# Optimization experiments

Measured on AMD Instinct MI355X. Metric: run time of the kernel, lower is better.

Reference implementation:

```python
import jax, jax.numpy as jnp
import numpy as np

N_NODES = 100000
N_EDGES = 1600000
F_IN, F1, F2, F3 = 128, 128, 128, 64


def setup_inputs() -> dict:
    key = jax.random.key(0)
    ks = jax.random.split(key, 10)
    edge_index = jax.random.randint(ks[0], (2, N_EDGES), 0, N_NODES, dtype=jnp.int64)
    x = jax.random.normal(ks[1], (N_NODES, F_IN), dtype=jnp.float32)
    def glorot(k, fi, fo):
        s = (6.0 / (fi + fo)) ** 0.5
        return jax.random.uniform(k, (fi, fo), jnp.float32, -s, s)
    return {
        "edge_index": edge_index,
        "x": x,
        "W1": glorot(ks[2], F_IN, F1), "b1": jnp.zeros((F1,), jnp.float32),
        "W2": glorot(ks[3], F1, F2), "b2": jnp.zeros((F2,), jnp.float32),
        "W3": glorot(ks[4], F2, F3), "b3": jnp.zeros((F3,), jnp.float32),
        "W_att": glorot(ks[5], F3, F3),
    }


def _gcn_conv(x, W, b, src, dst, deg_inv_sqrt):
    h = x @ W  # [N, Fo]
    norm = deg_inv_sqrt[src] * deg_inv_sqrt[dst]  # [E]
    agg = jax.ops.segment_sum(h[src] * norm[:, None], dst, num_segments=x.shape[0])
    agg = agg + h * (deg_inv_sqrt * deg_inv_sqrt)[:, None]  # self-loop term
    return agg + b


def _attention_pool(emb, W_att):
    # SimGNN attention pooling
    ctx = jnp.tanh(jnp.mean(emb @ W_att, axis=0))          # [F3]
    scores = jax.nn.sigmoid(emb @ ctx)                      # [N]
    return emb.T @ scores[:, None]                          # [F3, 1]


def reference(edge_index, x, W1, b1, W2, b2, W3, b3, W_att):
    src, dst = edge_index[0], edge_index[1]
    n = x.shape[0]
    deg = jax.ops.segment_sum(jnp.ones_like(src, dtype=x.dtype), dst, num_segments=n) + 1.0
    dis = jax.lax.rsqrt(deg)
    h = jax.nn.relu(_gcn_conv(x, W1, b1, src, dst, dis))
    h = jax.nn.relu(_gcn_conv(h, W2, b2, src, dst, dis))
    h = _gcn_conv(h, W3, b3, src, dst, dis)                 # abstract_features [N, F3]
    pooled = _attention_pool(h, W_att)                      # [F3, 1]
    return h, pooled
```

## Files before the change

kernel.cpp:

```cpp
#include <hip/hip_runtime.h>
#include <hip/hip_bf16.h>

#define NN 100000
#define NE 1600000
#define NR 100032
#define NB2 196
#define NBLK 391
#define EPB 4096

#if defined(__has_builtin)
#  if __has_builtin(__builtin_amdgcn_cvt_pk_f32_fp8) && \
      __has_builtin(__builtin_amdgcn_cvt_pk_fp8_f32) && \
      __has_builtin(__builtin_amdgcn_cvt_f32_fp8)
#    define HWF8 1
#  endif
#endif

typedef float f32x2 __attribute__((ext_vector_type(2)));
typedef float f32x4 __attribute__((ext_vector_type(4)));
typedef short bf16x8 __attribute__((ext_vector_type(8)));

static __device__ __forceinline__ float bf2f(__hip_bfloat16 v) { return __bfloat162float(v); }
static __device__ __forceinline__ float bfu(unsigned short w) {
    return __uint_as_float((unsigned)w << 16);
}

static __device__ __forceinline__ float f8d_sw(unsigned b) {
    unsigned e = (b >> 3) & 15u, m = b & 7u;
    float mag;
    if (e == 0) mag = (float)m * 0.001953125f;
    else        mag = __uint_as_float(((e + 120u) << 23) | (m << 20));
    return (b & 0x80u) ? -mag : mag;
}
static __device__ __forceinline__ unsigned char f8e_sw(float x) {
    unsigned u = __float_as_uint(x);
    unsigned s = (u >> 31) << 7;
    unsigned au = u & 0x7fffffffu;
    if (au >= 0x43E00000u) return (unsigned char)(s | 0x7Eu);
    if (au <  0x3A800000u) return (unsigned char)s;
    if (au <  0x3C800000u) {
        float a = __uint_as_float(au);
        int m = (int)rintf(a * 512.0f);
        if (m >= 8) return (unsigned char)(s | 0x08u);
        return (unsigned char)(s | (unsigned)m);
    }
    au += 0x80000u;
    if (au >= 0x43E00000u) return (unsigned char)(s | 0x7Eu);
    unsigned e = (au >> 23) - 120u;
    unsigned m = (au >> 20) & 7u;
    return (unsigned char)(s | (e << 3) | m);
}

static __device__ __forceinline__ void f8d4(unsigned u, float* o) {
#ifdef HWF8
    f32x2 lo = __builtin_amdgcn_cvt_pk_f32_fp8((int)u, false);
    f32x2 hi = __builtin_amdgcn_cvt_pk_f32_fp8((int)u, true);
    o[0] = lo.x; o[1] = lo.y; o[2] = hi.x; o[3] = hi.y;
#else
    o[0] = f8d_sw(u & 255u); o[1] = f8d_sw((u >> 8) & 255u);
    o[2] = f8d_sw((u >> 16) & 255u); o[3] = f8d_sw(u >> 24);
#endif
}
static __device__ __forceinline__ unsigned short f8e2(float a, float b) {
#ifdef HWF8
    float ca = fminf(fmaxf(a, -448.0f), 448.0f);
    float cb = fminf(fmaxf(b, -448.0f), 448.0f);
    int p = __builtin_amdgcn_cvt_pk_fp8_f32(ca, cb, 0, false);
    return (unsigned short)(p & 0xFFFF);
#else
    return (unsigned short)f8e_sw(a) | ((unsigned short)f8e_sw(b) << 8);
#endif
}
static __device__ __forceinline__ unsigned bfpack(float lo, float hi) {
    return (__float_as_uint(lo) >> 16) | (__float_as_uint(hi) & 0xFFFF0000u);
}

static __device__ __forceinline__ void acc8_add(f32x2* acc, uint2 v) {
#ifdef HWF8
    acc[0] += __builtin_amdgcn_cvt_pk_f32_fp8((int)v.x, false);
    acc[1] += __builtin_amdgcn_cvt_pk_f32_fp8((int)v.x, true);
    acc[2] += __builtin_amdgcn_cvt_pk_f32_fp8((int)v.y, false);
    acc[3] += __builtin_amdgcn_cvt_pk_f32_fp8((int)v.y, true);
#else
    unsigned u[2] = {v.x, v.y};
#pragma unroll
    for (int q = 0; q < 2; q++) {
        float o[4]; f8d4(u[q], o);
        acc[2 * q]     += (f32x2){o[0], o[1]};
        acc[2 * q + 1] += (f32x2){o[2], o[3]};
    }
#endif
}

__global__ void k_probe1(const unsigned short* __restrict__ xw,
                         const int* __restrict__ ei, int* __restrict__ raw) {
    int i = blockIdx.x * 256 + threadIdx.x;
    int nan = ((xw[i] & 0x7F80u) == 0x7F80u) ? 1 : 0;
    int odd = (ei[2 * i + 1] != 0) ? 1 : 0;
    unsigned long long bn = __ballot(nan);
    unsigned long long bo = __ballot(odd);
    if ((threadIdx.x & 63) == 0) {
        if (bn) atomicAdd(&raw[0], __popcll(bn));
        if (bo) atomicAdd(&raw[1], __popcll(bo));
    }
}

static __device__ __forceinline__ int e_src(const int* ei, int e, int f64) {
    int v = f64 ? ei[2 * e] : ei[e];
    return min(max(v, 0), NN - 1);
}
static __device__ __forceinline__ int e_dst(const int* ei, int e, int f64) {
    int v = f64 ? ei[2 * (NE + e)] : ei[NE + e];
    return min(max(v, 0), NN - 1);
}
static __device__ __forceinline__ float ldx(const void* p, long long i, int f32) {
    return f32 ? ((const float*)p)[i] : bf2f(((const __hip_bfloat16*)p)[i]);
}

__global__ __launch_bounds__(256) void k_prep(const void* __restrict__ x,
                                              const void* W1, const void* b1,
                                              const void* W2, const void* b2,
                                              const void* W3, const void* b3,
                                              const void* Wa,
                                              unsigned short* W1b, unsigned short* W2b,
                                              unsigned short* W3b,
                                              float* b1f, float* b2f, float* b3f,
                                              float* Waf,
                                              unsigned char* __restrict__ P,
                                              const int* __restrict__ raw,
                                              float* colsum, float* pooled, int* wsync) {
    int t = threadIdx.x;
    int gi = blockIdx.x;
    int f = raw[0] > 0;
    if (gi < 12500) {
        int i = gi * 256 + t;
        unsigned pk;
        if (f) {
            float4 v = ((const float4*)x)[i];
            pk = (unsigned)f8e2(v.x, v.y) | ((unsigned)f8e2(v.z, v.w) << 16);
        } else {
            ushort4 v = ((const ushort4*)x)[i];
            pk = (unsigned)f8e2(bfu(v.x), bfu(v.y)) | ((unsigned)f8e2(bfu(v.z), bfu(v.w)) << 16);
        }
        ((unsigned*)P)[i] = pk;
        return;
    }
    int i = (gi - 12500) * 256 + t;
    {
        int j = i & 7, l = (i >> 3) & 63, c = (i >> 9) & 7, kc = i >> 12;
        int k = kc * 32 + ((l >> 4)) * 8 + j;
        int col = c * 16 + (l & 15);
        W1b[i] = __bfloat16_as_ushort(__float2bfloat16(ldx(W1, k * 128 + col, f)));
        W2b[i] = __bfloat16_as_ushort(__float2bfloat16(ldx(W2, k * 128 + col, f)));
    }
    if (i < 8192) {
        int j = i & 7, l = (i >> 3) & 63, c = (i >> 9) & 3, kc = i >> 11;
        int k = kc * 32 + ((l >> 4)) * 8 + j;
        int col = c * 16 + (l & 15);
        W3b[i] = __bfloat16_as_ushort(__float2bfloat16(ldx(W3, k * 64 + col, f)));
    }
    if (i < 4096)  Waf[i] = ldx(Wa, i, f);
    if (i < 128)   { b1f[i] = ldx(b1, i, f); b2f[i] = ldx(b2, i, f); }
    if (i < 64)    b3f[i] = ldx(b3, i, f);
    if (gi == 12500) {
        if (t < 64) { colsum[t] = 0.0f; pooled[t] = 0.0f; }
        if (t == 0) *wsync = 0;
    }
    if (gi == 12501) {
        for (int z = t; z < (NR - NN) * 32; z += 256)
            ((unsigned*)(P + (size_t)NN * 128))[z] = 0u;
    }
}

__global__ __launch_bounds__(256) void k_hist(const int* __restrict__ ei,
                                              int* __restrict__ ghist,
                                              const int* __restrict__ raw) {
    __shared__ int h[NB2];
    int blk = blockIdx.x, t = threadIdx.x;
    for (int i = t; i < NB2; i += 256) h[i] = 0;
    __syncthreads();
    int f64 = (raw[1] == 0);
    int e0 = blk * EPB;
    for (int i = t; i < EPB; i += 256) {
        int e = e0 + i;
        if (e < NE) atomicAdd(&h[e_dst(ei, e, f64) >> 9], 1);
    }
    __syncthreads();
    for (int i = t; i < NB2; i += 256) ghist[blk * NB2 + i] = h[i];
}

__global__ __launch_bounds__(256) void k_off(const int* __restrict__ ghist,
                                             int* __restrict__ cbase,
                                             int* __restrict__ offm,
                                             int* __restrict__ rowptr) {
    __shared__ int tot[NB2];
    int t = threadIdx.x;
    if (t < NB2) {
        int s = 0;
        for (int blk = 0; blk < NBLK; blk++) s += ghist[blk * NB2 + t];
        tot[t] = s;
    }
    __syncthreads();
    if (t == 0) {
        int run = 0;
        for (int b = 0; b < NB2; b++) { cbase[b] = run; run += tot[b]; }
        cbase[NB2] = run;
        rowptr[NN] = run;
    }
    __syncthreads();
    if (t < NB2) {
        int run = cbase[t];
        for (int blk = 0; blk < NBLK; blk++) {
            offm[blk * NB2 + t] = run;
            run += ghist[blk * NB2 + t];
        }
    }
}

__global__ __launch_bounds__(256) void k_scatter(const int* __restrict__ ei,
                                                 const int* __restrict__ offm,
                                                 int* __restrict__ scratch,
                                                 const int* __restrict__ raw) {
    __shared__ int cur[NB2];
    int blk = blockIdx.x, t = threadIdx.x;
    for (int i = t; i < NB2; i += 256) cur[i] = offm[blk * NB2 + i];
    __syncthreads();
    int f64 = (raw[1] == 0);
    int e0 = blk * EPB;
    for (int i = t; i < EPB; i += 256) {
        int e = e0 + i;
        if (e < NE) {
            int d = e_dst(ei, e, f64);
            int s = e_src(ei, e, f64);
            int p = atomicAdd(&cur[d >> 9], 1);
            p = min(max(p, 0), NE - 1);
            scratch[p] = s | ((d & 511) << 17);
        }
    }
}

__global__ __launch_bounds__(256) void k_build(const int* __restrict__ scratch,
                                               const int* __restrict__ cbase,
                                               int* __restrict__ rowptr,
                                               float* __restrict__ dis,
                                               int* __restrict__ csr) {
    __shared__ int hist[512];
    __shared__ int base[512];
    __shared__ int sd[256];
    int b = blockIdx.x, t = threadIdx.x;
    int n0 = b << 9;
    int s0 = cbase[b], s1 = cbase[b + 1];
    hist[t] = 0; hist[t + 256] = 0;
    __syncthreads();
    for (int i = s0 + t; i < s1; i += 256) {
        int dlo = (scratch[i] >> 17) & 511;
        atomicAdd(&hist[dlo], 1);
    }
    __syncthreads();
    int v0 = hist[2 * t], v1 = hist[2 * t + 1];
    int s = v0 + v1;
    sd[t] = s; __syncthreads();
    for (int o = 1; o < 256; o <<= 1) {
        int add = (t >= o) ? sd[t - o] : 0;
        __syncthreads();
        sd[t] += add;
        __syncthreads();
    }
    int run = s0 + sd[t] - s;
    base[2 * t] = run;
    base[2 * t + 1] = run + v0;
    int n = n0 + 2 * t;
    if (n < NN) {
        rowptr[n] = run;
        dis[n] = rsqrtf((float)v0 + 1.0f);
    }
    if (n + 1 < NN) {
        rowptr[n + 1] = run + v0;
        dis[n + 1] = rsqrtf((float)v1 + 1.0f);
    }
    __syncthreads();
    for (int i = s0 + t; i < s1; i += 256) {
        int v = scratch[i];
        int dlo = (v >> 17) & 511;
        int p = atomicAdd(&base[dlo], 1);
        p = min(max(p, 0), NE - 1);
        csr[p] = v & 0x1FFFF;
    }
}

template <int NCT>
__global__ __launch_bounds__(256) void k_xf_mfma(const unsigned char* __restrict__ A,
                                                 const unsigned short* __restrict__ Wf,
                                                 const float* __restrict__ dis,
                                                 unsigned char* __restrict__ O) {
    __shared__ unsigned short wl[NCT * 4 * 64 * 8];
    int t = threadIdx.x;
    int n0 = blockIdx.x * 64;
    {
        const uint4* wg = (const uint4*)Wf;
        uint4* wld = (uint4*)wl;
#pragma unroll
        for (int i = 0; i < NCT; i++) wld[i * 256 + t] = wg[i * 256 + t];
    }
    __syncthreads();
    int w = t >> 6, l = t & 63;
    int quad = l >> 4, m = l & 15;
    int node = n0 + w * 16 + m;
    const unsigned char* ap = A + (size_t)node * 128 + quad * 8;
    f32x4 acc[NCT];
#pragma unroll
    for (int c = 0; c < NCT; c++) acc[c] = (f32x4){0.0f, 0.0f, 0.0f, 0.0f};
#pragma unroll
    for (int kc = 0; kc < 4; kc++) {
        uint2 g = *(const uint2*)(ap + kc * 32);
        float o[8];
        f8d4(g.x, o); f8d4(g.y, o + 4);
        union { unsigned u[4]; bf16x8 v; } fr;
        fr.u[0] = bfpack(o[0], o[1]);
        fr.u[1] = bfpack(o[2], o[3]);
        fr.u[2] = bfpack(o[4], o[5]);
        fr.u[3] = bfpack(o[6], o[7]);
#pragma unroll
        for (int c = 0; c < NCT; c++) {
            bf16x8 bw = *(const bf16x8*)&wl[((kc * NCT + c) * 64 + l) * 8];
            acc[c] = __builtin_amdgcn_mfma_f32_16x16x32_bf16(bw, fr.v, acc[c], 0, 0, 0);
        }
    }
    float d = (node < NN) ? dis[node] : 0.0f;
    if (node <= NN) {
        unsigned char* orow = O + (size_t)node * (NCT * 16) + quad * 4;
#pragma unroll
        for (int c = 0; c < NCT; c++) {
            unsigned pk = (unsigned)f8e2(acc[c][0] * d, acc[c][1] * d)
                        | ((unsigned)f8e2(acc[c][2] * d, acc[c][3] * d) << 16);
            *(unsigned*)(orow + c * 16) = pk;
        }
    }
}

template <bool RELU>
__global__ __launch_bounds__(256) void k_agg128(const unsigned char* __restrict__ Tb,
                                                const int* __restrict__ rowptr,
                                                const int* __restrict__ csr,
                                                const float* __restrict__ dis,
                                                const float* __restrict__ bias,
                                                unsigned char* __restrict__ H) {
    int n = blockIdx.x * 4 + (threadIdx.x >> 6);
    int lane = threadIdx.x & 63;
    int r = lane >> 4;
    int f = lane & 15;
    int fo = f << 3;
    float dn = dis[n];
    int s0 = rowptr[n], s1 = rowptr[n + 1];
    s0 = min(max(s0, 0), NE); s1 = min(max(s1, s0), NE);
    f32x2 acc[4];
#pragma unroll
    for (int k = 0; k < 4; k++) acc[k] = (f32x2){0.0f, 0.0f};
    if (r == 0) {
        uint2 v = *(const uint2*)(Tb + (((unsigned)n << 7) + (unsigned)fo));
        acc8_add(acc, v);
    }
    for (int base = s0; base < s1; base += 64) {
        int m = min(64, s1 - base);
        unsigned voff = (unsigned)NN << 7;
        if (lane < m) voff = (unsigned)csr[base + lane] << 7;
        int nq = (m + 15) >> 4;
        for (int q = 0; q < nq; q++) {
            int a0 = q * 64 + r * 4;
            unsigned vo0 = (unsigned)__builtin_amdgcn_ds_bpermute(a0,      (int)voff);
            unsigned vo1 = (unsigned)__builtin_amdgcn_ds_bpermute(a0 + 16, (int)voff);
            unsigned vo2 = (unsigned)__builtin_amdgcn_ds_bpermute(a0 + 32, (int)voff);
            unsigned vo3 = (unsigned)__builtin_amdgcn_ds_bpermute(a0 + 48, (int)voff);
            uint2 v0 = *(const uint2*)(Tb + (vo0 + (unsigned)fo));
            uint2 v1 = *(const uint2*)(Tb + (vo1 + (unsigned)fo));
            uint2 v2 = *(const uint2*)(Tb + (vo2 + (unsigned)fo));
            uint2 v3 = *(const uint2*)(Tb + (vo3 + (unsigned)fo));
            acc8_add(acc, v0);
            acc8_add(acc, v1);
            acc8_add(acc, v2);
            acc8_add(acc, v3);
        }
    }
#pragma unroll
    for (int k = 0; k < 4; k++) {
        acc[k].x += __shfl_xor(acc[k].x, 16, 64);
        acc[k].y += __shfl_xor(acc[k].y, 16, 64);
        acc[k].x += __shfl_xor(acc[k].x, 32, 64);
        acc[k].y += __shfl_xor(acc[k].y, 32, 64);
    }
    if (r == 0) {
        float4 bA = *(const float4*)(bias + fo);
        float4 bB = *(const float4*)(bias + fo + 4);
        float t[8];
        t[0] = acc[0].x * dn + bA.x; t[1] = acc[0].y * dn + bA.y;
        t[2] = acc[1].x * dn + bA.z; t[3] = acc[1].y * dn + bA.w;
        t[4] = acc[2].x * dn + bB.x; t[5] = acc[2].y * dn + bB.y;
        t[6] = acc[3].x * dn + bB.z; t[7] = acc[3].y * dn + bB.w;
        if (RELU) {
#pragma unroll
            for (int k = 0; k < 8; k++) t[k] = fmaxf(t[k], 0.0f);
        }
        unsigned lo = (unsigned)f8e2(t[0], t[1]) | ((unsigned)f8e2(t[2], t[3]) << 16);
        unsigned hi = (unsigned)f8e2(t[4], t[5]) | ((unsigned)f8e2(t[6], t[7]) << 16);
        *(uint2*)(H + (((size_t)n << 7) + (size_t)fo)) = make_uint2(lo, hi);
    }
}

__global__ __launch_bounds__(256) void k_agg64(const unsigned char* __restrict__ Tb,
                                               const int* __restrict__ rowptr,
                                               const int* __restrict__ csr,
                                               const float* __restrict__ dis,
                                               const float* __restrict__ bias,
                                               unsigned short* __restrict__ Hb) {
    int lane = threadIdx.x & 63;
    int half = lane >> 5;
    int hl = lane & 31;
    int n = blockIdx.x * 8 + (threadIdx.x >> 6) * 2 + half;
    int r = hl >> 3;
    int f = hl & 7;
    int fo = f << 3;
    float dn = dis[n];
    int s0 = rowptr[n], s1 = rowptr[n + 1];
    s0 = min(max(s0, 0), NE); s1 = min(max(s1, s0), NE);
    f32x2 acc[4];
#pragma unroll
    for (int k = 0; k < 4; k++) acc[k] = (f32x2){0.0f, 0.0f};
    if (r == 0) {
        uint2 v = *(const uint2*)(Tb + (((unsigned)n << 6) + (unsigned)fo));
        acc8_add(acc, v);
    }
    int ab = half << 7;
    for (int base = s0; base < s1; base += 32) {
        int m = min(32, s1 - base);
        unsigned voff = (unsigned)NN << 6;
        if (hl < m) voff = (unsigned)csr[base + hl] << 6;
        int nq = (m + 15) >> 4;
        for (int q = 0; q < nq; q++) {
            int a0 = ab + q * 64 + r * 4;
            unsigned vo0 = (unsigned)__builtin_amdgcn_ds_bpermute(a0,      (int)voff);
            unsigned vo1 = (unsigned)__builtin_amdgcn_ds_bpermute(a0 + 16, (int)voff);
            unsigned vo2 = (unsigned)__builtin_amdgcn_ds_bpermute(a0 + 32, (int)voff);
            unsigned vo3 = (unsigned)__builtin_amdgcn_ds_bpermute(a0 + 48, (int)voff);
            uint2 v0 = *(const uint2*)(Tb + (vo0 + (unsigned)fo));
            uint2 v1 = *(const uint2*)(Tb + (vo1 + (unsigned)fo));
            uint2 v2 = *(const uint2*)(Tb + (vo2 + (unsigned)fo));
            uint2 v3 = *(const uint2*)(Tb + (vo3 + (unsigned)fo));
            acc8_add(acc, v0);
            acc8_add(acc, v1);
            acc8_add(acc, v2);
            acc8_add(acc, v3);
        }
    }
#pragma unroll
    for (int k = 0; k < 4; k++) {
        acc[k].x += __shfl_xor(acc[k].x, 8, 64);
        acc[k].y += __shfl_xor(acc[k].y, 8, 64);
        acc[k].x += __shfl_xor(acc[k].x, 16, 64);
        acc[k].y += __shfl_xor(acc[k].y, 16, 64);
    }
    if (r == 0) {
        float4 bA = *(const float4*)(bias + fo);
        float4 bB = *(const float4*)(bias + fo + 4);
        float t[8];
        t[0] = acc[0].x * dn + bA.x; t[1] = acc[0].y * dn + bA.y;
        t[2] = acc[1].x * dn + bA.z; t[3] = acc[1].y * dn + bA.w;
        t[4] = acc[2].x * dn + bB.x; t[5] = acc[2].y * dn + bB.y;
        t[6] = acc[3].x * dn + bB.z; t[7] = acc[3].y * dn + bB.w;
        unsigned p0 = (unsigned)__bfloat16_as_ushort(__float2bfloat16(t[0])) |
                      ((unsigned)__bfloat16_as_ushort(__float2bfloat16(t[1])) << 16);
        unsigned p1 = (unsigned)__bfloat16_as_ushort(__float2bfloat16(t[2])) |
                      ((unsigned)__bfloat16_as_ushort(__float2bfloat16(t[3])) << 16);
        unsigned p2 = (unsigned)__bfloat16_as_ushort(__float2bfloat16(t[4])) |
                      ((unsigned)__bfloat16_as_ushort(__float2bfloat16(t[5])) << 16);
        unsigned p3 = (unsigned)__bfloat16_as_ushort(__float2bfloat16(t[6])) |
                      ((unsigned)__bfloat16_as_ushort(__float2bfloat16(t[7])) << 16);
        *(uint4*)(Hb + (((size_t)n << 6) + (size_t)fo)) = make_uint4(p0, p1, p2, p3);
    }
}

__global__ __launch_bounds__(512) void k_colsum(const unsigned short* __restrict__ h3,
                                                float* __restrict__ colsum,
                                                const float* __restrict__ Waf,
                                                float* __restrict__ ctx,
                                                int* __restrict__ wsync) {
    int t = threadIdx.x;
    int lane = t & 63;
    int rg = lane >> 4, cq = lane & 15;
    int wid = (blockIdx.x * 512 + t) >> 6;
    int nw = (gridDim.x * 512) >> 6;
    float a0 = 0, a1 = 0, a2 = 0, a3 = 0;
    for (int r = wid * 4 + rg; r < NN; r += nw * 4) {
        uint2 v = *(const uint2*)(h3 + ((size_t)r << 6) + cq * 4);
        a0 += bfu((unsigned short)(v.x & 0xFFFF));
        a1 += bfu((unsigned short)(v.x >> 16));
        a2 += bfu((unsigned short)(v.y & 0xFFFF));
        a3 += bfu((unsigned short)(v.y >> 16));
    }
    a0 += __shfl_xor(a0, 16, 64); a0 += __shfl_xor(a0, 32, 64);
    a1 += __shfl_xor(a1, 16, 64); a1 += __shfl_xor(a1, 32, 64);
    a2 += __shfl_xor(a2, 16, 64); a2 += __shfl_xor(a2, 32, 64);
    a3 += __shfl_xor(a3, 16, 64); a3 += __shfl_xor(a3, 32, 64);
    __shared__ float part[8][64];
    int w = t >> 6;
    if (rg == 0) {
        part[w][cq * 4 + 0] = a0;
        part[w][cq * 4 + 1] = a1;
        part[w][cq * 4 + 2] = a2;
        part[w][cq * 4 + 3] = a3;
    }
    __syncthreads();
    if (t < 64) {
        float s = 0;
#pragma unroll
        for (int i = 0; i < 8; i++) s += part[i][t];
        atomicAdd(&colsum[t], s);
    }
    __shared__ int lastf;
    __syncthreads();
    if (t == 0) {
        __threadfence();
        int old = atomicAdd(wsync, 1);
        lastf = (old == (int)gridDim.x - 1) ? 1 : 0;
    }
    __syncthreads();
    if (lastf) {
        __shared__ float ms[64];
        if (t < 64) {
            __threadfence();
            ms[t] = atomicAdd(&colsum[t], 0.0f) * (1.0f / NN);
        }
        __syncthreads();
        if (t < 64) {
            float s = 0.0f;
#pragma unroll
            for (int k = 0; k < 64; k++) s += ms[k] * Waf[k * 64 + t];
            ctx[t] = tanhf(s);
        }
    }
}

__global__ __launch_bounds__(512) void k_pool(const unsigned short* __restrict__ h3,
                                              const float* __restrict__ ctx,
                                              float* __restrict__ pooled,
                                              void* __restrict__ out,
                                              const int* __restrict__ raw) {
    int t = threadIdx.x;
    int lane = t & 63;
    int rg = lane >> 4, cq = lane & 15;
    int wid = (blockIdx.x * 512 + t) >> 6;
    int nw = (gridDim.x * 512) >> 6;
    int f32o = raw[0] > 0;
    float c0 = ctx[cq * 4 + 0], c1 = ctx[cq * 4 + 1];
    float c2 = ctx[cq * 4 + 2], c3 = ctx[cq * 4 + 3];
    float q0 = 0, q1 = 0, q2 = 0, q3 = 0;
    for (int r = wid * 4 + rg; r < NN; r += nw * 4) {
        uint2 v = *(const uint2*)(h3 + ((size_t)r << 6) + cq * 4);
        float x0 = bfu((unsigned short)(v.x & 0xFFFF));
        float x1 = bfu((unsigned short)(v.x >> 16));
        float x2 = bfu((unsigned short)(v.y & 0xFFFF));
        float x3 = bfu((unsigned short)(v.y >> 16));
        if (f32o) {
            *(float4*)((float*)out + ((size_t)r << 6) + cq * 4) =
                make_float4(x0, x1, x2, x3);
        } else {
            *(uint2*)((unsigned short*)out + ((size_t)r << 6) + cq * 4) = v;
        }
        float p = x0 * c0 + x1 * c1 + x2 * c2 + x3 * c3;
        p += __shfl_xor(p, 1, 64);
        p += __shfl_xor(p, 2, 64);
        p += __shfl_xor(p, 4, 64);
        p += __shfl_xor(p, 8, 64);
        float sc = 1.0f / (1.0f + expf(-p));
        q0 += sc * x0; q1 += sc * x1; q2 += sc * x2; q3 += sc * x3;
    }
    q0 += __shfl_xor(q0, 16, 64); q0 += __shfl_xor(q0, 32, 64);
    q1 += __shfl_xor(q1, 16, 64); q1 += __shfl_xor(q1, 32, 64);
    q2 += __shfl_xor(q2, 16, 64); q2 += __shfl_xor(q2, 32, 64);
    q3 += __shfl_xor(q3, 16, 64); q3 += __shfl_xor(q3, 32, 64);
    __shared__ float part[8][64];
    int w = t >> 6;
    if (rg == 0) {
        part[w][cq * 4 + 0] = q0;
        part[w][cq * 4 + 1] = q1;
        part[w][cq * 4 + 2] = q2;
        part[w][cq * 4 + 3] = q3;
    }
    __syncthreads();
    if (t < 64) {
        float s = 0;
#pragma unroll
        for (int i = 0; i < 8; i++) s += part[i][t];
        atomicAdd(&pooled[t], s);
    }
}

__global__ void k_tail(const float* __restrict__ pooled, void* __restrict__ out,
                       const int* __restrict__ raw) {
    int j = threadIdx.x;
    if (raw[0] > 0) {
        ((float*)out)[6400000 + j] = pooled[j];
    } else {
        ((unsigned short*)out)[6400000 + j] =
            __bfloat16_as_ushort(__float2bfloat16(pooled[j]));
    }
}

static constexpr size_t AL(size_t x) { return (x + 255) & ~size_t(255); }
static constexpr size_t OFF_FLAGS  = 0;
static constexpr size_t OFF_RAW    = OFF_FLAGS + 256;
static constexpr size_t OFF_GHIST  = OFF_RAW + 256;
static constexpr size_t OFF_OFFM   = OFF_GHIST + AL((size_t)NBLK * NB2 * 4);
static constexpr size_t OFF_CBASE  = OFF_OFFM + AL((size_t)NBLK * NB2 * 4);
static constexpr size_t OFF_ROWPTR = OFF_CBASE + AL((NB2 + 1) * 4);
static constexpr size_t OFF_CSR    = OFF_ROWPTR + AL((NN + 1) * 4);
static constexpr size_t OFF_DIS    = OFF_CSR + AL((size_t)NE * 4);
static constexpr size_t OFF_P      = OFF_DIS + AL(NN * 4);
static constexpr size_t OFF_W1B    = OFF_P + AL((size_t)NR * 128);
static constexpr size_t OFF_W2B    = OFF_W1B + AL(16384 * 2);
static constexpr size_t OFF_W3B    = OFF_W2B + AL(16384 * 2);
static constexpr size_t OFF_B1F    = OFF_W3B + AL(8192 * 2);
static constexpr size_t OFF_B2F    = OFF_B1F + AL(128 * 4);
static constexpr size_t OFF_B3F    = OFF_B2F + AL(128 * 4);
static constexpr size_t OFF_WAF    = OFF_B3F + AL(64 * 4);
static constexpr size_t OFF_COLSUM = OFF_WAF + AL(4096 * 4);
static constexpr size_t OFF_POOLED = OFF_COLSUM + AL(64 * 4);
static constexpr size_t OFF_CTX    = OFF_POOLED + AL(64 * 4);
static constexpr size_t OFF_SYNC   = OFF_CTX + AL(64 * 4);

extern "C" void kernel_launch(void* const* d_in, const int* in_sizes, int n_in,
                              void* d_out, int out_size, void* d_ws, size_t ws_size,
                              hipStream_t stream) {
    const int* ei = (const int*)d_in[0];
    const void* x  = d_in[1];
    const void* W1 = d_in[2];
    const void* b1 = d_in[3];
    const void* W2 = d_in[4];
    const void* b2 = d_in[5];
    const void* W3 = d_in[6];
    const void* b3 = d_in[7];
    const void* Wa = d_in[8];

    char* ws = (char*)d_ws;
    int*   raw    = (int*)(ws + OFF_RAW);
    int*   ghist  = (int*)(ws + OFF_GHIST);
    int*   offm   = (int*)(ws + OFF_OFFM);
    int*   cbase  = (int*)(ws + OFF_CBASE);
    int*   rowptr = (int*)(ws + OFF_ROWPTR);
    int*   csr    = (int*)(ws + OFF_CSR);
    float* dis    = (float*)(ws + OFF_DIS);
    unsigned char*  P    = (unsigned char*)(ws + OFF_P);
    int*            scrA = (int*)(ws + OFF_P);
    unsigned short* Hb   = (unsigned short*)(ws + OFF_P);
    unsigned short* W1b = (unsigned short*)(ws + OFF_W1B);
    unsigned short* W2b = (unsigned short*)(ws + OFF_W2B);
    unsigned short* W3b = (unsigned short*)(ws + OFF_W3B);
    float* b1f    = (float*)(ws + OFF_B1F);
    float* b2f    = (float*)(ws + OFF_B2F);
    float* b3f    = (float*)(ws + OFF_B3F);
    float* Waf    = (float*)(ws + OFF_WAF);
    float* colsum = (float*)(ws + OFF_COLSUM);
    float* pooled = (float*)(ws + OFF_POOLED);
    float* ctx    = (float*)(ws + OFF_CTX);
    int*   wsync  = (int*)(ws + OFF_SYNC);

    unsigned char* Q = (unsigned char*)d_out;

    hipMemsetAsync(raw, 0, 256, stream);

    k_probe1<<<256, 256, 0, stream>>>((const unsigned short*)x, ei, raw);

    k_hist<<<NBLK, 256, 0, stream>>>(ei, ghist, raw);
    k_off<<<1, 256, 0, stream>>>(ghist, cbase, offm, rowptr);
    k_scatter<<<NBLK, 256, 0, stream>>>(ei, offm, scrA, raw);
    k_build<<<NB2, 256, 0, stream>>>(scrA, cbase, rowptr, dis, csr);

    k_prep<<<12564, 256, 0, stream>>>(x, W1, b1, W2, b2, W3, b3, Wa,
                                      W1b, W2b, W3b, b1f, b2f, b3f, Waf,
                                      P, raw, colsum, pooled, wsync);

    k_xf_mfma<8><<<NR / 64, 256, 0, stream>>>(P, W1b, dis, Q);
    k_agg128<true><<<NN / 4, 256, 0, stream>>>(Q, rowptr, csr, dis, b1f, P);
    k_xf_mfma<8><<<NR / 64, 256, 0, stream>>>(P, W2b, dis, Q);
    k_agg128<true><<<NN / 4, 256, 0, stream>>>(Q, rowptr, csr, dis, b2f, P);
    k_xf_mfma<4><<<NR / 64, 256, 0, stream>>>(P, W3b, dis, Q);
    k_agg64<<<NN / 8, 256, 0, stream>>>(Q, rowptr, csr, dis, b3f, Hb);

    k_colsum<<<256, 512, 0, stream>>>(Hb, colsum, Waf, ctx, wsync);
    k_pool<<<256, 512, 0, stream>>>(Hb, ctx, pooled, d_out, raw);
    k_tail<<<1, 64, 0, stream>>>(pooled, d_out, raw);
}
```

Baseline: 393.1 us.

## Parallelize bucket offset scan across blocks and fold pool tail into k_pool

Replaces the single-block serial offset computation with a per-bucket parallel wave scan over histogram blocks plus a tiny serial kernel for bucket bases. k_scatter now adds the bucket base itself. Writing the pooled output is moved into k_pool's last-finishing block via an atomic counter, removing a separate launch. This targets the long serial latency chain in the old k_off at the cost of an extra small kernel and last-block synchronisation.

```diff
diff --git a/kernel.cpp b/kernel.cpp
--- a/kernel.cpp
+++ b/kernel.cpp
@@ -164,7 +164,7 @@
     if (i < 64)    b3f[i] = ldx(b3, i, f);
     if (gi == 12500) {
         if (t < 64) { colsum[t] = 0.0f; pooled[t] = 0.0f; }
-        if (t == 0) *wsync = 0;
+        if (t == 0) { wsync[0] = 0; wsync[1] = 0; }
     }
     if (gi == 12501) {
         for (int z = t; z < (NR - NN) * 32; z += 256)
@@ -189,41 +189,51 @@
     for (int i = t; i < NB2; i += 256) ghist[blk * NB2 + i] = h[i];
 }
 
-__global__ __launch_bounds__(256) void k_off(const int* __restrict__ ghist,
-                                             int* __restrict__ cbase,
-                                             int* __restrict__ offm,
-                                             int* __restrict__ rowptr) {
-    __shared__ int tot[NB2];
+__global__ __launch_bounds__(512) void k_offA(const int* __restrict__ ghist,
+                                              int* __restrict__ tot,
+                                              int* __restrict__ offm) {
+    int b = blockIdx.x;
     int t = threadIdx.x;
-    if (t < NB2) {
-        int s = 0;
-        for (int blk = 0; blk < NBLK; blk++) s += ghist[blk * NB2 + t];
-        tot[t] = s;
-    }
+    __shared__ int wsum[8];
+    __shared__ int woff[8];
+    int v = (t < NBLK) ? ghist[t * NB2 + b] : 0;
+    int s = v;
+#pragma unroll
+    for (int o = 1; o < 64; o <<= 1) {
+        int u = __shfl_up(s, o, 64);
+        if ((t & 63) >= o) s += u;
+    }
+    int w = t >> 6;
+    if ((t & 63) == 63) wsum[w] = s;
     __syncthreads();
     if (t == 0) {
+        int run = 0;
+#pragma unroll
+        for (int i = 0; i < 8; i++) { woff[i] = run; run += wsum[i]; }
+        tot[b] = run;
+    }
+    __syncthreads();
+    if (t < NBLK) offm[t * NB2 + b] = s - v + woff[w];
+}
+
+__global__ void k_offB(const int* __restrict__ tot,
+                       int* __restrict__ cbase, int* __restrict__ rowptr) {
+    if (threadIdx.x == 0) {
         int run = 0;
         for (int b = 0; b < NB2; b++) { cbase[b] = run; run += tot[b]; }
         cbase[NB2] = run;
         rowptr[NN] = run;
     }
-    __syncthreads();
-    if (t < NB2) {
-        int run = cbase[t];
-        for (int blk = 0; blk < NBLK; blk++) {
-            offm[blk * NB2 + t] = run;
-            run += ghist[blk * NB2 + t];
-        }
-    }
 }
 
 __global__ __launch_bounds__(256) void k_scatter(const int* __restrict__ ei,
                                                  const int* __restrict__ offm,
+                                                 const int* __restrict__ cbase,
                                                  int* __restrict__ scratch,
                                                  const int* __restrict__ raw) {
     __shared__ int cur[NB2];
     int blk = blockIdx.x, t = threadIdx.x;
-    for (int i = t; i < NB2; i += 256) cur[i] = offm[blk * NB2 + i];
+    for (int i = t; i < NB2; i += 256) cur[i] = offm[blk * NB2 + i] + cbase[i];
     __syncthreads();
     int f64 = (raw[1] == 0);
     int e0 = blk * EPB;
@@ -519,7 +529,7 @@
     __syncthreads();
     if (t == 0) {
         __threadfence();
-        int old = atomicAdd(wsync, 1);
+        int old = atomicAdd(&wsync[0], 1);
         lastf = (old == (int)gridDim.x - 1) ? 1 : 0;
     }
     __syncthreads();
@@ -543,7 +553,8 @@
                                               const float* __restrict__ ctx,
                                               float* __restrict__ pooled,
                                               void* __restrict__ out,
-                                              const int* __restrict__ raw) {
+                                              const int* __restrict__ raw,
+                                              int* __restrict__ wsync) {
     int t = threadIdx.x;
     int lane = t & 63;
     int rg = lane >> 4, cq = lane & 15;
@@ -592,16 +603,23 @@
         for (int i = 0; i < 8; i++) s += part[i][t];
         atomicAdd(&pooled[t], s);
     }
-}
-
-__global__ void k_tail(const float* __restrict__ pooled, void* __restrict__ out,
-                       const int* __restrict__ raw) {
-    int j = threadIdx.x;
-    if (raw[0] > 0) {
-        ((float*)out)[6400000 + j] = pooled[j];
-    } else {
-        ((unsigned short*)out)[6400000 + j] =
-            __bfloat16_as_ushort(__float2bfloat16(pooled[j]));
+    __shared__ int lastf;
+    __syncthreads();
+    if (t == 0) {
+        __threadfence();
+        int old = atomicAdd(&wsync[1], 1);
+        lastf = (old == (int)gridDim.x - 1) ? 1 : 0;
+    }
+    __syncthreads();
+    if (lastf && t < 64) {
+        __threadfence();
+        float pv = atomicAdd(&pooled[t], 0.0f);
+        if (f32o) {
+            ((float*)out)[6400000 + t] = pv;
+        } else {
+            ((unsigned short*)out)[6400000 + t] =
+                __bfloat16_as_ushort(__float2bfloat16(pv));
+        }
     }
 }
 
@@ -626,6 +644,7 @@
 static constexpr size_t OFF_POOLED = OFF_COLSUM + AL(64 * 4);
 static constexpr size_t OFF_CTX    = OFF_POOLED + AL(64 * 4);
 static constexpr size_t OFF_SYNC   = OFF_CTX + AL(64 * 4);
+static constexpr size_t OFF_TOT    = OFF_SYNC + 256;
 
 extern "C" void kernel_launch(void* const* d_in, const int* in_sizes, int n_in,
                               void* d_out, int out_size, void* d_ws, size_t ws_size,
@@ -662,6 +681,7 @@
     float* pooled = (float*)(ws + OFF_POOLED);
     float* ctx    = (float*)(ws + OFF_CTX);
     int*   wsync  = (int*)(ws + OFF_SYNC);
+    int*   tot    = (int*)(ws + OFF_TOT);
 
     unsigned char* Q = (unsigned char*)d_out;
 
@@ -670,8 +690,9 @@
     k_probe1<<<256, 256, 0, stream>>>((const unsigned short*)x, ei, raw);
 
     k_hist<<<NBLK, 256, 0, stream>>>(ei, ghist, raw);
-    k_off<<<1, 256, 0, stream>>>(ghist, cbase, offm, rowptr);
-    k_scatter<<<NBLK, 256, 0, stream>>>(ei, offm, scrA, raw);
+    k_offA<<<NB2, 512, 0, stream>>>(ghist, tot, offm);
+    k_offB<<<1, 64, 0, stream>>>(tot, cbase, rowptr);
+    k_scatter<<<NBLK, 256, 0, stream>>>(ei, offm, cbase, scrA, raw);
     k_build<<<NB2, 256, 0, stream>>>(scrA, cbase, rowptr, dis, csr);
 
     k_prep<<<12564, 256, 0, stream>>>(x, W1, b1, W2, b2, W3, b3, Wa,
@@ -686,6 +707,5 @@
     k_agg64<<<NN / 8, 256, 0, stream>>>(Q, rowptr, csr, dis, b3f, Hb);
 
     k_colsum<<<256, 512, 0, stream>>>(Hb, colsum, Waf, ctx, wsync);
-    k_pool<<<256, 512, 0, stream>>>(Hb, ctx, pooled, d_out, raw);
-    k_tail<<<1, 64, 0, stream>>>(pooled, d_out, raw);
-}
+    k_pool<<<256, 512, 0, stream>>>(Hb, ctx, pooled, d_out, raw, wsync);
+}
```

New measurement: 367.3 us. 1.07x faster.
